# Optimization experiments

Hardware: AMD Instinct MI355X
Metric: run time of the kernel (lower is better)

Reference implementation:

```python
import jax, jax.numpy as jnp
import numpy as np

N_QUBITS = 12
DEPTH = 6
BATCH = 4096

# Wire 0 is the most-significant bit (PennyLane default.qubit convention).

def _rx(t):
    c = jnp.cos(t / 2).astype(jnp.complex64)
    s = (-1j * jnp.sin(t / 2)).astype(jnp.complex64)
    return jnp.stack([jnp.stack([c, s], -1), jnp.stack([s, c], -1)], -2)

def _ry(t):
    c = jnp.cos(t / 2).astype(jnp.complex64)
    s = jnp.sin(t / 2).astype(jnp.complex64)
    return jnp.stack([jnp.stack([c, -s], -1), jnp.stack([s, c], -1)], -2)

def _rz(t):
    em = jnp.exp(-1j * t.astype(jnp.complex64) / 2)
    ep = jnp.exp(1j * t.astype(jnp.complex64) / 2)
    z = jnp.zeros_like(em)
    return jnp.stack([jnp.stack([em, z], -1), jnp.stack([z, ep], -1)], -2)

def _apply_1q(state, gate, q, n):
    # state: (B, 2^n); gate: (2,2) shared or (B,2,2) batched
    B = state.shape[0]
    st = state.reshape(B, 1 << q, 2, 1 << (n - 1 - q))
    eq = 'ab,xlbr->xlar' if gate.ndim == 2 else 'xab,xlbr->xlar'
    return jnp.einsum(eq, gate, st).reshape(B, -1)

def _apply_cnot(state, c, n):
    # CNOT with control c, target c+1 (adjacent wires)
    B = state.shape[0]
    st = state.reshape(B, 1 << c, 2, 2, 1 << (n - 2 - c))
    st = jnp.concatenate([st[:, :, 0:1], st[:, :, 1:2, ::-1]], axis=2)
    return st.reshape(B, -1)

def _z_signs(n):
    idx = jnp.arange(1 << n)
    bits = (idx[None, :] >> (n - 1 - jnp.arange(n))[:, None]) & 1  # (n, 2^n)
    return (1.0 - 2.0 * bits).astype(jnp.float32)

def setup_inputs() -> dict:
    key = jax.random.key(0)
    k1, k2 = jax.random.split(key)
    x = jax.random.normal(k1, (BATCH, N_QUBITS), dtype=jnp.float32)
    params = jax.random.normal(k2, (DEPTH, N_QUBITS, 3), dtype=jnp.float32)
    return {"x": x, "params": params}

def reference(x, params):
    B, n = x.shape
    depth = params.shape[0]
    state = jnp.zeros((B, 1 << n), jnp.complex64).at[:, 0].set(1.0)
    # input encoding: batched RX per qubit
    for i in range(n):
        state = _apply_1q(state, _rx(x[:, i]), i, n)
    for d in range(depth):
        for i in range(n):
            state = _apply_1q(state, _ry(params[d, i, 0]), i, n)
            state = _apply_1q(state, _rz(params[d, i, 1]), i, n)
            state = _apply_1q(state, _rx(params[d, i, 2]), i, n)
        for i in range(n - 1):
            state = _apply_cnot(state, i, n)
    probs = state.real ** 2 + state.imag ** 2  # (B, 2^n)
    return probs @ _z_signs(n).T  # (B, n) Pauli-Z expvals
```

## Files before the change

kernel.cpp:

```cpp
#include <hip/hip_runtime.h>

#define NQ    12
#define DIM   4096
#define DEPTH 6
#define BLK   256
#define RJ    16


__device__ __forceinline__ int fsw(int q) { return q ^ ((q >> 5) & 31); }

__device__ __host__ __forceinline__ constexpr int sufxc(int v) {
  v ^= v >> 1; v ^= v >> 2; v ^= v >> 4; v ^= v >> 8; return v;
}
__device__ __host__ __forceinline__ constexpr int K1c(int j) {
  const int q = j << 4; return q ^ ((q >> 5) & 31);
}
__device__ __host__ __forceinline__ constexpr int K2c(int j) {
  const int q = j << 8; return q ^ ((q >> 5) & 31);
}
__device__ __host__ __forceinline__ constexpr int KCc(int j) {
  const int hi = (sufxc(j) & 15) << 8;
  const int lo = (__builtin_popcount((unsigned)j) & 1) ? 0xFF : 0;
  const int c  = hi | lo;
  return c ^ ((c >> 5) & 31);
}

template <int B>
__device__ __forceinline__ void gate4(float (&re)[RJ], float (&im)[RJ],
                                      float4 u0, float4 u1) {
  const float u00r = u0.x, u00i = u0.y, u01r = u0.z, u01i = u0.w;
  const float u10r = u1.x, u10i = u1.y, u11r = u1.z, u11i = u1.w;
#pragma unroll
  for (int m = 0; m < RJ / 2; ++m) {
    const int lo = m & ((1 << B) - 1);
    const int j0 = ((m >> B) << (B + 1)) | lo;
    const int j1 = j0 | (1 << B);
    const float ar = re[j0], ai = im[j0];
    const float br = re[j1], bi = im[j1];
    float nr0 = u00r * ar; nr0 = fmaf(-u00i, ai, nr0); nr0 = fmaf(u01r, br, nr0); nr0 = fmaf(-u01i, bi, nr0);
    float ni0 = u00r * ai; ni0 = fmaf( u00i, ar, ni0); ni0 = fmaf(u01r, bi, ni0); ni0 = fmaf( u01i, br, ni0);
    float nr1 = u10r * ar; nr1 = fmaf(-u10i, ai, nr1); nr1 = fmaf(u11r, br, nr1); nr1 = fmaf(-u11i, bi, nr1);
    float ni1 = u10r * ai; ni1 = fmaf( u10i, ar, ni1); ni1 = fmaf(u11r, bi, ni1); ni1 = fmaf( u11i, br, ni1);
    re[j0] = nr0; im[j0] = ni0;
    re[j1] = nr1; im[j1] = ni1;
  }
}

__global__ __launch_bounds__(BLK) void qsim_kernel(const float* __restrict__ x,
                                                   const float* __restrict__ params,
                                                   float* __restrict__ out) {
  __shared__ float sm[2 * DIM];
  __shared__ float uTab[DEPTH * NQ * 8];

  const int T = threadIdx.x;
  const int b = blockIdx.x;

  if (T < DEPTH * NQ) {
    const int d = T / NQ, w = T % NQ;
    const float py = params[T * 3 + 0];
    const float pz = params[T * 3 + 1];
    const float px = params[T * 3 + 2];
    float sa, ca, sb, cb, sg, cg;
    __sincosf(py * 0.5f, &sa, &ca);
    __sincosf(pz * 0.5f, &sb, &cb);
    __sincosf(px * 0.5f, &sg, &cg);
    const float Ar = ca * cb, Ai = -ca * sb;
    const float Br = -sa * cb, Bi = sa * sb;
    const float Cr = sa * cb, Ci = sa * sb;
    const float Dr = ca * cb, Di = ca * sb;
    float* u = &uTab[(d * NQ + w) * 8];
    u[0] = cg * Ar + sg * Ci;   u[1] = cg * Ai - sg * Cr;
    u[2] = cg * Br + sg * Di;   u[3] = cg * Bi - sg * Dr;
    u[4] = sg * Ai + cg * Cr;   u[5] = -sg * Ar + cg * Ci;
    u[6] = sg * Bi + cg * Dr;   u[7] = -sg * Br + cg * Di;
  }

  float re[RJ], im[RJ];
  {
    float cs[NQ], sn[NQ];
#pragma unroll
    for (int i = 0; i < NQ; ++i) __sincosf(x[b * NQ + i] * 0.5f, &sn[i], &cs[i]);
    float hm = 1.0f;
#pragma unroll
    for (int i = 0; i < 8; ++i) hm *= ((T >> (7 - i)) & 1) ? sn[i] : cs[i];
    re[0] = hm;
#pragma unroll
    for (int bb = 0; bb < 4; ++bb) {
#pragma unroll
      for (int j = 0; j < (1 << bb); ++j) {
        re[j | (1 << bb)] = re[j] * sn[11 - bb];
        re[j] = re[j] * cs[11 - bb];
      }
    }
    const int pt = __popc(T);
#pragma unroll
    for (int j = 0; j < RJ; ++j) {
      const float m = re[j];
      const int k = (pt + __popc(j)) & 3;
      re[j] = (k & 1) ? 0.0f : ((k & 2) ? -m : m);
      im[j] = (k & 1) ? ((k & 2) ? m : -m) : 0.0f;
    }
  }

  __syncthreads();

  const int A0 = fsw(T << 4);
  const int B0 = fsw(((T >> 4) << 8) | (T & 15));
  const int C0 = fsw(T);
  const int D0 = fsw(sufxc(T) & 255);

#define SWEEP(D, WBASE)                                                       \
  {                                                                           \
    const float4* uv0 = (const float4*)&uTab[((D) * NQ + (WBASE)) * 8];       \
    gate4<0>(re, im, uv0[0], uv0[1]);                                         \
    const float4* uv1 = (const float4*)&uTab[((D) * NQ + (WBASE) - 1) * 8];   \
    gate4<1>(re, im, uv1[0], uv1[1]);                                         \
    const float4* uv2 = (const float4*)&uTab[((D) * NQ + (WBASE) - 2) * 8];   \
    gate4<2>(re, im, uv2[0], uv2[1]);                                         \
    const float4* uv3 = (const float4*)&uTab[((D) * NQ + (WBASE) - 3) * 8];   \
    gate4<3>(re, im, uv3[0], uv3[1]);                                         \
  }
#define ST_ALL(EXPR)                                                          \
  {                                                                           \
    _Pragma("unroll") for (int j = 0; j < RJ; ++j) {                          \
      const int a_ = (EXPR);                                                  \
      sm[a_] = re[j]; sm[DIM + a_] = im[j];                                   \
    }                                                                         \
  }
#define LD_ALL(EXPR)                                                          \
  {                                                                           \
    _Pragma("unroll") for (int j = 0; j < RJ; ++j) {                          \
      const int a_ = (EXPR);                                                  \
      re[j] = sm[a_]; im[j] = sm[DIM + a_];                                   \
    }                                                                         \
  }

#pragma unroll 1
  for (int d = 0; d < DEPTH; ++d) {
    SWEEP(d, 11)
    ST_ALL(A0 ^ j) __syncthreads();
    LD_ALL(B0 ^ K1c(j)) __syncthreads();
    SWEEP(d, 7)
    ST_ALL(B0 ^ K1c(j)) __syncthreads();
    LD_ALL(C0 ^ K2c(j)) __syncthreads();
    SWEEP(d, 3)
    ST_ALL(D0 ^ KCc(j)) __syncthreads();
    LD_ALL(A0 ^ j) __syncthreads();
  }
#undef SWEEP
#undef ST_ALL
#undef LD_ALL

  float tot = 0.f, s0 = 0.f, s1 = 0.f, s2 = 0.f, s3 = 0.f;
#pragma unroll
  for (int j = 0; j < RJ; ++j) {
    const float p = fmaf(re[j], re[j], im[j] * im[j]);
    tot += p;
    s0 += (j & 1) ? -p : p;
    s1 += (j & 2) ? -p : p;
    s2 += (j & 4) ? -p : p;
    s3 += (j & 8) ? -p : p;
  }
  float v[NQ];
#pragma unroll
  for (int w = 0; w < 8; ++w) v[w] = ((T >> (7 - w)) & 1) ? -tot : tot;
  v[8] = s3; v[9] = s2; v[10] = s1; v[11] = s0;
#pragma unroll
  for (int w = 0; w < NQ; ++w) {
#pragma unroll
    for (int o = 32; o > 0; o >>= 1) v[w] += __shfl_xor(v[w], o);
  }
  const int wv = T >> 6, lt = T & 63;
  if (lt == 0) {
#pragma unroll
    for (int w = 0; w < NQ; ++w) sm[w * 4 + wv] = v[w];
  }
  __syncthreads();
  if (T < NQ) out[b * NQ + T] = (sm[T * 4 + 0] + sm[T * 4 + 1]) +
                                (sm[T * 4 + 2] + sm[T * 4 + 3]);
}

extern "C" void kernel_launch(void* const* d_in, const int* in_sizes, int n_in,
                              void* d_out, int out_size, void* d_ws, size_t ws_size,
                              hipStream_t stream) {
  const float* x      = (const float*)d_in[0];
  const float* params = (const float*)d_in[1];
  float* out          = (float*)d_out;
  const int B = in_sizes[0] / NQ;
  qsim_kernel<<<B, BLK, 0, stream>>>(x, params, out);
}
```

Baseline: 255.1 us.

## Pack amplitudes as float2 for packed FMA and 64-bit LDS access

After: 242.5 us. 5.0% less time.

```diff
diff --git a/kernel.cpp b/kernel.cpp
--- a/kernel.cpp
+++ b/kernel.cpp
@@ -7,56 +7,58 @@
 #define RJ    16
 
 
-__device__ __forceinline__ int fsw(int q) { return q ^ ((q >> 5) & 31); }
+typedef float f32x2 __attribute__((ext_vector_type(2)));
 
 __device__ __host__ __forceinline__ constexpr int sufxc(int v) {
   v ^= v >> 1; v ^= v >> 2; v ^= v >> 4; v ^= v >> 8; return v;
 }
-__device__ __host__ __forceinline__ constexpr int K1c(int j) {
-  const int q = j << 4; return q ^ ((q >> 5) & 31);
+__device__ __host__ __forceinline__ constexpr int K1w(int j) { return (j << 4) ^ j; }
+__device__ __host__ __forceinline__ constexpr int K2w(int j) { return j << 8; }
+__device__ __host__ __forceinline__ constexpr int KCw(int j) {
+  const int s4 = sufxc(j) & 15;
+  const int p  = __builtin_popcount((unsigned)j) & 1;
+  return (s4 << 8) | (p ? 0xF0 : 0);
 }
-__device__ __host__ __forceinline__ constexpr int K2c(int j) {
-  const int q = j << 8; return q ^ ((q >> 5) & 31);
-}
-__device__ __host__ __forceinline__ constexpr int KCc(int j) {
-  const int hi = (sufxc(j) & 15) << 8;
-  const int lo = (__builtin_popcount((unsigned)j) & 1) ? 0xFF : 0;
-  const int c  = hi | lo;
-  return c ^ ((c >> 5) & 31);
+
+__device__ __forceinline__ f32x2 pfma(f32x2 a, f32x2 b, f32x2 c) {
+  return __builtin_elementwise_fma(a, b, c);
 }
 
 template <int B>
-__device__ __forceinline__ void gate4(float (&re)[RJ], float (&im)[RJ],
-                                      float4 u0, float4 u1) {
-  const float u00r = u0.x, u00i = u0.y, u01r = u0.z, u01i = u0.w;
-  const float u10r = u1.x, u10i = u1.y, u11r = u1.z, u11i = u1.w;
+__device__ __forceinline__ void gate4(f32x2 (&amp)[RJ], float4 u0, float4 u1) {
+  const f32x2 r00 = {u0.x, u0.x}, mi00 = {-u0.y, u0.y};
+  const f32x2 r01 = {u0.z, u0.z}, mi01 = {-u0.w, u0.w};
+  const f32x2 r10 = {u1.x, u1.x}, mi10 = {-u1.y, u1.y};
+  const f32x2 r11 = {u1.z, u1.z}, mi11 = {-u1.w, u1.w};
 #pragma unroll
   for (int m = 0; m < RJ / 2; ++m) {
     const int lo = m & ((1 << B) - 1);
     const int j0 = ((m >> B) << (B + 1)) | lo;
     const int j1 = j0 | (1 << B);
-    const float ar = re[j0], ai = im[j0];
-    const float br = re[j1], bi = im[j1];
-    float nr0 = u00r * ar; nr0 = fmaf(-u00i, ai, nr0); nr0 = fmaf(u01r, br, nr0); nr0 = fmaf(-u01i, bi, nr0);
-    float ni0 = u00r * ai; ni0 = fmaf( u00i, ar, ni0); ni0 = fmaf(u01r, bi, ni0); ni0 = fmaf( u01i, br, ni0);
-    float nr1 = u10r * ar; nr1 = fmaf(-u10i, ai, nr1); nr1 = fmaf(u11r, br, nr1); nr1 = fmaf(-u11i, bi, nr1);
-    float ni1 = u10r * ai; ni1 = fmaf( u10i, ar, ni1); ni1 = fmaf(u11r, bi, ni1); ni1 = fmaf( u11i, br, ni1);
-    re[j0] = nr0; im[j0] = ni0;
-    re[j1] = nr1; im[j1] = ni1;
+    const f32x2 a = amp[j0], b = amp[j1];
+    const f32x2 ax = a.yx, bx = b.yx;
+    f32x2 n0 = r00 * a;
+    n0 = pfma(mi00, ax, n0);
+    n0 = pfma(r01, b, n0);
+    n0 = pfma(mi01, bx, n0);
+    f32x2 n1 = r10 * a;
+    n1 = pfma(mi10, ax, n1);
+    n1 = pfma(r11, b, n1);
+    n1 = pfma(mi11, bx, n1);
+    amp[j0] = n0; amp[j1] = n1;
   }
 }
 
 __global__ __launch_bounds__(BLK) void qsim_kernel(const float* __restrict__ x,
                                                    const float* __restrict__ params,
                                                    float* __restrict__ out) {
-  __shared__ float sm[2 * DIM];
+  __shared__ f32x2 sm2[DIM];
   __shared__ float uTab[DEPTH * NQ * 8];
 
   const int T = threadIdx.x;
   const int b = blockIdx.x;
 
   if (T < DEPTH * NQ) {
-    const int d = T / NQ, w = T % NQ;
     const float py = params[T * 3 + 0];
     const float pz = params[T * 3 + 1];
     const float px = params[T * 3 + 2];
@@ -68,14 +70,14 @@
     const float Br = -sa * cb, Bi = sa * sb;
     const float Cr = sa * cb, Ci = sa * sb;
     const float Dr = ca * cb, Di = ca * sb;
-    float* u = &uTab[(d * NQ + w) * 8];
+    float* u = &uTab[T * 8];
     u[0] = cg * Ar + sg * Ci;   u[1] = cg * Ai - sg * Cr;
     u[2] = cg * Br + sg * Di;   u[3] = cg * Bi - sg * Dr;
     u[4] = sg * Ai + cg * Cr;   u[5] = -sg * Ar + cg * Ci;
     u[6] = sg * Bi + cg * Dr;   u[7] = -sg * Br + cg * Di;
   }
 
-  float re[RJ], im[RJ];
+  f32x2 amp[RJ];
   {
     float cs[NQ], sn[NQ];
 #pragma unroll
@@ -83,69 +85,66 @@
     float hm = 1.0f;
 #pragma unroll
     for (int i = 0; i < 8; ++i) hm *= ((T >> (7 - i)) & 1) ? sn[i] : cs[i];
-    re[0] = hm;
+    float mag[RJ];
+    mag[0] = hm;
 #pragma unroll
     for (int bb = 0; bb < 4; ++bb) {
 #pragma unroll
       for (int j = 0; j < (1 << bb); ++j) {
-        re[j | (1 << bb)] = re[j] * sn[11 - bb];
-        re[j] = re[j] * cs[11 - bb];
+        mag[j | (1 << bb)] = mag[j] * sn[11 - bb];
+        mag[j] = mag[j] * cs[11 - bb];
       }
     }
     const int pt = __popc(T);
 #pragma unroll
     for (int j = 0; j < RJ; ++j) {
-      const float m = re[j];
+      const float m = mag[j];
       const int k = (pt + __popc(j)) & 3;
-      re[j] = (k & 1) ? 0.0f : ((k & 2) ? -m : m);
-      im[j] = (k & 1) ? ((k & 2) ? m : -m) : 0.0f;
+      const float rr = (k & 1) ? 0.0f : ((k & 2) ? -m : m);
+      const float ii = (k & 1) ? ((k & 2) ? m : -m) : 0.0f;
+      amp[j] = (f32x2){rr, ii};
     }
   }
 
   __syncthreads();
 
-  const int A0 = fsw(T << 4);
-  const int B0 = fsw(((T >> 4) << 8) | (T & 15));
-  const int C0 = fsw(T);
-  const int D0 = fsw(sufxc(T) & 255);
+  const int A0w = (T << 4) ^ (T & 15);
+  const int B0w = ((T >> 4) << 8) | (T & 15);
+  const int C0w = T ^ ((T >> 4) & 15);
+  const int CT  = sufxc(T) & 255;
+  const int D0w = CT ^ ((CT >> 4) & 15);
 
 #define SWEEP(D, WBASE)                                                       \
   {                                                                           \
     const float4* uv0 = (const float4*)&uTab[((D) * NQ + (WBASE)) * 8];       \
-    gate4<0>(re, im, uv0[0], uv0[1]);                                         \
+    gate4<0>(amp, uv0[0], uv0[1]);                                            \
     const float4* uv1 = (const float4*)&uTab[((D) * NQ + (WBASE) - 1) * 8];   \
-    gate4<1>(re, im, uv1[0], uv1[1]);                                         \
+    gate4<1>(amp, uv1[0], uv1[1]);                                            \
     const float4* uv2 = (const float4*)&uTab[((D) * NQ + (WBASE) - 2) * 8];   \
-    gate4<2>(re, im, uv2[0], uv2[1]);                                         \
+    gate4<2>(amp, uv2[0], uv2[1]);                                            \
     const float4* uv3 = (const float4*)&uTab[((D) * NQ + (WBASE) - 3) * 8];   \
-    gate4<3>(re, im, uv3[0], uv3[1]);                                         \
+    gate4<3>(amp, uv3[0], uv3[1]);                                            \
   }
 #define ST_ALL(EXPR)                                                          \
   {                                                                           \
-    _Pragma("unroll") for (int j = 0; j < RJ; ++j) {                          \
-      const int a_ = (EXPR);                                                  \
-      sm[a_] = re[j]; sm[DIM + a_] = im[j];                                   \
-    }                                                                         \
+    _Pragma("unroll") for (int j = 0; j < RJ; ++j) { sm2[(EXPR)] = amp[j]; }  \
   }
 #define LD_ALL(EXPR)                                                          \
   {                                                                           \
-    _Pragma("unroll") for (int j = 0; j < RJ; ++j) {                          \
-      const int a_ = (EXPR);                                                  \
-      re[j] = sm[a_]; im[j] = sm[DIM + a_];                                   \
-    }                                                                         \
+    _Pragma("unroll") for (int j = 0; j < RJ; ++j) { amp[j] = sm2[(EXPR)]; }  \
   }
 
 #pragma unroll 1
   for (int d = 0; d < DEPTH; ++d) {
     SWEEP(d, 11)
-    ST_ALL(A0 ^ j) __syncthreads();
-    LD_ALL(B0 ^ K1c(j)) __syncthreads();
+    ST_ALL(A0w ^ j) __syncthreads();
+    LD_ALL(B0w ^ K1w(j)) __syncthreads();
     SWEEP(d, 7)
-    ST_ALL(B0 ^ K1c(j)) __syncthreads();
-    LD_ALL(C0 ^ K2c(j)) __syncthreads();
+    ST_ALL(B0w ^ K1w(j)) __syncthreads();
+    LD_ALL(C0w ^ K2w(j)) __syncthreads();
     SWEEP(d, 3)
-    ST_ALL(D0 ^ KCc(j)) __syncthreads();
-    LD_ALL(A0 ^ j) __syncthreads();
+    ST_ALL(D0w ^ KCw(j)) __syncthreads();
+    LD_ALL(A0w ^ j) __syncthreads();
   }
 #undef SWEEP
 #undef ST_ALL
@@ -154,7 +153,7 @@
   float tot = 0.f, s0 = 0.f, s1 = 0.f, s2 = 0.f, s3 = 0.f;
 #pragma unroll
   for (int j = 0; j < RJ; ++j) {
-    const float p = fmaf(re[j], re[j], im[j] * im[j]);
+    const float p = fmaf(amp[j].x, amp[j].x, amp[j].y * amp[j].y);
     tot += p;
     s0 += (j & 1) ? -p : p;
     s1 += (j & 2) ? -p : p;
@@ -171,13 +170,14 @@
     for (int o = 32; o > 0; o >>= 1) v[w] += __shfl_xor(v[w], o);
   }
   const int wv = T >> 6, lt = T & 63;
+  float* smf = (float*)sm2;
   if (lt == 0) {
 #pragma unroll
-    for (int w = 0; w < NQ; ++w) sm[w * 4 + wv] = v[w];
+    for (int w = 0; w < NQ; ++w) smf[w * 4 + wv] = v[w];
   }
   __syncthreads();
-  if (T < NQ) out[b * NQ + T] = (sm[T * 4 + 0] + sm[T * 4 + 1]) +
-                                (sm[T * 4 + 2] + sm[T * 4 + 3]);
+  if (T < NQ) out[b * NQ + T] = (smf[T * 4 + 0] + smf[T * 4 + 1]) +
+                                (smf[T * 4 + 2] + smf[T * 4 + 3]);
 }
 
 extern "C" void kernel_launch(void* const* d_in, const int* in_sizes, int n_in,
```
